# Kernel tuning notes

Measured on AMD Instinct MI355X. Metric: run time of the kernel, lower is better.

## Reference

```python
import jax, jax.numpy as jnp
import numpy as np
from jax import lax

N = 20000          # num_nodes_total
N_GHOST = 2000     # nodes with mask == 0
T_IN = 8
FEAT = 16          # node_features
HID = 128          # hidden_dim
E = 320000         # edges (~avg degree 16)
D = 2              # downstream_concat_depth
ALPHA = 0.5        # alpha_boundary
FUSER_IN = FEAT * (1 + D) + 1   # 49
FUSER_H = max(32, 2 * FEAT * (1 + D))  # 96
GATE_H = max(8, FUSER_H // 2)   # 48


def _lin(k, fan_in, shape):
    b = 1.0 / np.sqrt(fan_in)
    return jax.random.uniform(k, shape, jnp.float32, -b, b)


def setup_inputs() -> dict:
    key = jax.random.key(0)
    ks = jax.random.split(key, 26)
    x = jax.random.normal(ks[0], (N, T_IN, FEAT), jnp.float32)
    src = jax.random.randint(ks[1], (E,), 0, N, jnp.int32)
    dst = jax.random.randint(ks[2], (E,), 0, N, jnp.int32)
    # guarantee every ghost node (ids [0, N_GHOST)) has an outgoing edge to a real node
    src = src.at[:N_GHOST].set(jnp.arange(N_GHOST, dtype=jnp.int32))
    dst = dst.at[:N_GHOST].set(jax.random.randint(ks[3], (N_GHOST,), N_GHOST, N, jnp.int32))
    edge_index = jnp.stack([src, dst])
    edge_attr = jax.random.uniform(ks[4], (E, 1), jnp.float32, minval=0.05, maxval=2.0)
    mask = jnp.concatenate([jnp.zeros(N_GHOST, jnp.int32), jnp.ones(N - N_GHOST, jnp.int32)])
    H3 = 3 * HID
    return dict(
        x=x, edge_attr=edge_attr,
        W_lin=_lin(ks[5], FEAT, (FEAT, HID)), b_lin=_lin(ks[6], FEAT, (HID,)),
        Wc1=_lin(ks[7], HID, (HID, HID)), bc1=jnp.zeros((HID,), jnp.float32),
        Wc2=_lin(ks[8], HID, (HID, HID)), bc2=jnp.zeros((HID,), jnp.float32),
        W_ih=_lin(ks[9], HID, (HID, H3)), b_ih=_lin(ks[10], HID, (H3,)),
        W_hh=_lin(ks[11], HID, (HID, H3)), b_hh=_lin(ks[12], HID, (H3,)),
        Wf1=_lin(ks[13], FUSER_IN, (FUSER_IN, FUSER_H)), bf1=_lin(ks[14], FUSER_IN, (FUSER_H,)),
        Wf2=_lin(ks[15], FUSER_H, (FUSER_H, FEAT)), bf2=_lin(ks[16], FUSER_H, (FEAT,)),
        Wg1=_lin(ks[17], FUSER_IN, (FUSER_IN, GATE_H)), bg1=_lin(ks[18], FUSER_IN, (GATE_H,)),
        Wg2=_lin(ks[19], GATE_H, (GATE_H, 1)), bg2=_lin(ks[20], GATE_H, (1,)),
        edge_index=edge_index, mask=mask,
    )


def _forward(x, edge_attr, W_lin, b_lin, Wc1, bc1, Wc2, bc2, W_ih, b_ih, W_hh, b_hh,
             Wf1, bf1, Wf2, bf2, Wg1, bg1, Wg2, bg2, edge_index, mask):
    src, dst = edge_index[0], edge_index[1]
    ghost_idx = jnp.nonzero(mask == 0, size=N_GHOST)[0]
    dist = jnp.maximum(edge_attr[:, 0], 1e-6)                     # [E]
    # first outgoing edge per source node (earliest edge id per src, cf. argsort trick)
    eid = jnp.arange(E, dtype=jnp.int32)
    first_eid = jax.ops.segment_min(eid, src, num_segments=N)    # int32 max where no edge
    has = first_eid < E
    safe = jnp.where(has, first_eid, 0)
    first_out = jnp.where(has, dst[safe], -1)                     # [N]
    first_dx = jnp.where(has, dist[safe], -1.0)                   # [N]
    b_idx = first_out[ghost_idx]                                  # boundary node per ghost
    dx_bnd = jnp.maximum(first_dx[ghost_idx], 1e-6)[:, None]      # [G,1]
    # D downstream hops, staying put where no outgoing edge exists
    dK, cur = [], b_idx
    for _ in range(D):
        nxt = first_out[cur]
        nxt = jnp.where(nxt < 0, cur, nxt)
        dK.append(nxt)
        cur = nxt
    # GCN symmetric normalization with self-loops (PyG gcn_norm)
    deg = jnp.zeros((N,), x.dtype).at[dst].add(1.0) + 1.0         # in-degree + self-loop
    dis = deg ** -0.5
    norm_e = (dis[src] * dis[dst])[:, None]                       # [E,1]
    norm_self = (1.0 / deg)[:, None]                              # [N,1]

    def gcn(h, W, b):
        hw = h @ W                                                # [N,HID]
        agg = jnp.zeros_like(hw).at[dst].add(hw[src] * norm_e)    # scatter-add messages
        return agg + hw * norm_self + b

    def gru(g, h):
        gi = g @ W_ih + b_ih                                      # [N,3H]
        gh = h @ W_hh + b_hh
        ir, iz, inn = jnp.split(gi, 3, axis=1)
        hr, hz, hn = jnp.split(gh, 3, axis=1)
        r = jax.nn.sigmoid(ir + hr)
        z = jax.nn.sigmoid(iz + hz)
        n = jnp.tanh(inn + r * hn)
        return (1.0 - z) * n + z * h

    def step(h, x_t):
        gf = x_t[ghost_idx]                                       # [G,F]
        feats = jnp.concatenate([gf] + [x_t[i] for i in dK] + [dx_bnd], axis=1)  # [G,FUSER_IN]
        zf = jax.nn.relu(feats @ Wf1 + bf1)
        delta = zf @ Wf2 + bf2
        gate = jax.nn.sigmoid(jax.nn.relu(feats @ Wg1 + bg1) @ Wg2 + bg2)
        x_t = x_t.at[ghost_idx].set(gf + ALPHA * delta * gate)
        g = jax.nn.relu(x_t @ W_lin + b_lin)
        g = jax.nn.relu(gcn(g, Wc1, bc1))
        g = jax.nn.relu(gcn(g, Wc2, bc2))
        return gru(g, h), None

    h0 = jnp.zeros((N, HID), x.dtype)
    h, _ = lax.scan(step, h0, jnp.swapaxes(x, 0, 1))              # scan over T_IN
    return h


def reference(x, edge_attr, W_lin, b_lin, Wc1, bc1, Wc2, bc2, W_ih, b_ih, W_hh, b_hh,
              Wf1, bf1, Wf2, bf2, Wg1, bg1, Wg2, bg2, edge_index, mask):
    return _forward(x, edge_attr, W_lin, b_lin, Wc1, bc1, Wc2, bc2, W_ih, b_ih, W_hh, b_hh,
                    Wf1, bf1, Wf2, bf2, Wg1, bg1, Wg2, bg2, edge_index, mask)
```

## Files before the change

kernel.cpp:

```cpp
#include <hip/hip_runtime.h>
#include <math.h>

#define NN 20000
#define T_IN 8
#define FEAT 16
#define HID 128
#define H3 384
#define FUSER_IN 49
#define FUSER_H 96
#define GATE_H 48
#define ALPHA 0.5f

typedef unsigned short u16;
typedef __attribute__((ext_vector_type(8))) short bf16x8_t;
typedef __attribute__((ext_vector_type(4))) float f32x4_t;

__device__ __forceinline__ float sigmoidf_(float v) { return 1.0f / (1.0f + expf(-v)); }

__device__ __forceinline__ u16 f2b(float v) {
    unsigned u = __float_as_uint(v);
    unsigned r = (u + 0x7fffu + ((u >> 16) & 1u)) >> 16;
    return (u16)r;
}
__device__ __forceinline__ float b2f(u16 u) { return __uint_as_float(((unsigned)u) << 16); }


__global__ void init_kernel(int* first_eid, int* deg_cnt, int* gcount, int n) {
    int i = blockIdx.x * 256 + threadIdx.x;
    if (i < n) { first_eid[i] = 0x7fffffff; deg_cnt[i] = 0; }
    if (i == 0) *gcount = 0;
}

__global__ void edge_pass1(const int* __restrict__ src, const int* __restrict__ dst,
                           int* first_eid, int* deg_cnt, int e) {
    int i = blockIdx.x * 256 + threadIdx.x;
    if (i < e) {
        atomicMin(&first_eid[src[i]], i);
        atomicAdd(&deg_cnt[dst[i]], 1);
    }
}

__global__ void scan1(const int* __restrict__ cnt, int* tmp, int* bsum, int n) {
    __shared__ int buf[256];
    int tid = threadIdx.x;
    int i = blockIdx.x * 256 + tid;
    int v = (i < n) ? cnt[i] : 0;
    buf[tid] = v;
    __syncthreads();
    #pragma unroll
    for (int off = 1; off < 256; off <<= 1) {
        int t = (tid >= off) ? buf[tid - off] : 0;
        __syncthreads();
        buf[tid] += t;
        __syncthreads();
    }
    if (i < n) tmp[i] = buf[tid];
    if (tid == 255) bsum[blockIdx.x] = buf[255];
}

__global__ void scan2(int* bsum, int nb) {
    __shared__ int buf[256];
    int tid = threadIdx.x;
    int v = (tid < nb) ? bsum[tid] : 0;
    buf[tid] = v;
    __syncthreads();
    #pragma unroll
    for (int off = 1; off < 256; off <<= 1) {
        int t = (tid >= off) ? buf[tid - off] : 0;
        __syncthreads();
        buf[tid] += t;
        __syncthreads();
    }
    if (tid < nb) bsum[tid] = buf[tid];
}

__global__ void scan3(const int* __restrict__ cnt, const int* __restrict__ tmp,
                      const int* __restrict__ bsum,
                      int* row_ptr, int* fill_ptr, float* dis, float* norm_self, int n) {
    int i = blockIdx.x * 256 + threadIdx.x;
    if (i >= n) return;
    int pre = (blockIdx.x > 0) ? bsum[blockIdx.x - 1] : 0;
    int incl = tmp[i] + pre;
    int v = cnt[i];
    row_ptr[i + 1] = incl;
    fill_ptr[i] = incl - v;
    float deg = (float)v + 1.0f;
    dis[i] = 1.0f / sqrtf(deg);
    norm_self[i] = 1.0f / deg;
    if (i == 0) row_ptr[0] = 0;
}

__global__ void firsts_kernel(const int* __restrict__ first_eid, const int* __restrict__ dst,
                              const float* __restrict__ edge_attr,
                              int* first_out, float* first_dx, int n, int e) {
    int i = blockIdx.x * 256 + threadIdx.x;
    if (i >= n) return;
    int fe = first_eid[i];
    if (fe < e) {
        first_out[i] = dst[fe];
        first_dx[i] = fmaxf(edge_attr[fe], 1e-6f);
    } else {
        first_out[i] = -1;
        first_dx[i] = -1.0f;
    }
}

__global__ void edge_pass2(const int* __restrict__ src, const int* __restrict__ dst,
                           int* fill_ptr, const float* __restrict__ dis,
                           int* csr_src, float* csr_w, int e) {
    int i = blockIdx.x * 256 + threadIdx.x;
    if (i < e) {
        int d = dst[i], s = src[i];
        int pos = atomicAdd(&fill_ptr[d], 1);
        csr_src[pos] = s;
        csr_w[pos] = dis[s] * dis[d];
    }
}

__global__ void ghost_kernel(const int* __restrict__ mask, const int* __restrict__ first_out,
                             const float* __restrict__ first_dx,
                             int* d1_of, int* d2_of, float* dxb_of,
                             int* ghost_list, int* ghost_pos, int* gcount, int n) {
    int i = blockIdx.x * 256 + threadIdx.x;
    if (i >= n) return;
    if (mask[i] != 0) { ghost_pos[i] = -1; return; }
    int pos = atomicAdd(gcount, 1);
    ghost_list[pos] = i;
    ghost_pos[i] = pos;
    int b = first_out[i];
    float dxb = fmaxf(first_dx[i], 1e-6f);
    int d1, d2;
    if (b < 0) { d1 = i; d2 = i; }
    else {
        int n1 = first_out[b]; d1 = (n1 < 0) ? b : n1;
        int n2 = first_out[d1]; d2 = (n2 < 0) ? d1 : n2;
    }
    d1_of[i] = d1; d2_of[i] = d2; dxb_of[i] = dxb;
}

__global__ void zero2_kernel(float* a, int na, unsigned* b, int nb) {
    int stride = gridDim.x * 256;
    for (int i = blockIdx.x * 256 + threadIdx.x; i < na; i += stride) a[i] = 0.0f;
    for (int i = blockIdx.x * 256 + threadIdx.x; i < nb; i += stride) b[i] = 0u;
}

__global__ __launch_bounds__(256)
void wsplit_kernel(const float* __restrict__ W, u16* BT_hi, u16* BT_lo, int Ncols) {
    __shared__ float tile[32][33];
    int nb = blockIdx.x * 32;
    int kb = blockIdx.y * 32;
    int tx = threadIdx.x & 31, ty = threadIdx.x >> 5;
    #pragma unroll
    for (int r = 0; r < 32; r += 8)
        tile[ty + r][tx] = W[(size_t)(kb + ty + r) * Ncols + nb + tx];
    __syncthreads();
    #pragma unroll
    for (int r = 0; r < 32; r += 8) {
        float v = tile[tx][ty + r];
        u16 h = f2b(v);
        size_t off = (size_t)(nb + ty + r) * 128 + kb + tx;
        BT_hi[off] = h;
        BT_lo[off] = f2b(v - b2f(h));
    }
}


__global__ __launch_bounds__(128)
void fuse_ghost(const float* __restrict__ x,
                const int* __restrict__ ghost_list, const int* __restrict__ gcount,
                const int* __restrict__ d1_of, const int* __restrict__ d2_of,
                const float* __restrict__ dxb_of,
                const float* __restrict__ Wf1, const float* __restrict__ bf1,
                const float* __restrict__ Wf2, const float* __restrict__ bf2,
                const float* __restrict__ Wg1, const float* __restrict__ bg1,
                const float* __restrict__ Wg2, const float* __restrict__ bg2,
                float* __restrict__ xf_buf) {
    int slot = blockIdx.x;
    if (slot >= *gcount) return;
    int t = blockIdx.y;
    int i = ghost_list[slot];
    int j = threadIdx.x;
    __shared__ float feats[FUSER_IN];
    __shared__ float z1[FUSER_H];
    __shared__ float zg[GATE_H];
    __shared__ float s_gate;

    if (j < FEAT) {
        int d1 = d1_of[i], d2 = d2_of[i];
        feats[j]            = x[((size_t)i * T_IN + t) * FEAT + j];
        feats[FEAT + j]     = x[((size_t)d1 * T_IN + t) * FEAT + j];
        feats[2 * FEAT + j] = x[((size_t)d2 * T_IN + t) * FEAT + j];
    }
    if (j == 0) feats[3 * FEAT] = dxb_of[i];
    __syncthreads();
    if (j < FUSER_H) {
        float acc = bf1[j];
        for (int k = 0; k < FUSER_IN; ++k) acc = fmaf(feats[k], Wf1[k * FUSER_H + j], acc);
        z1[j] = fmaxf(acc, 0.0f);
    }
    if (j < GATE_H) {
        float acc = bg1[j];
        for (int k = 0; k < FUSER_IN; ++k) acc = fmaf(feats[k], Wg1[k * GATE_H + j], acc);
        zg[j] = fmaxf(acc, 0.0f);
    }
    __syncthreads();
    if (j == 0) {
        float s = bg2[0];
        for (int k = 0; k < GATE_H; ++k) s = fmaf(zg[k], Wg2[k], s);
        s_gate = sigmoidf_(s);
    }
    __syncthreads();
    if (j < FEAT) {
        float acc = bf2[j];
        for (int k = 0; k < FUSER_H; ++k) acc = fmaf(z1[k], Wf2[k * FEAT + j], acc);
        xf_buf[((size_t)slot * T_IN + t) * FEAT + j] = feats[j] + ALPHA * acc * s_gate;
    }
}

__global__ __launch_bounds__(256)
void lin_all(const float* __restrict__ x, const float* __restrict__ xf_buf,
             const int* __restrict__ ghost_pos,
             const float* __restrict__ W_lin, const float* __restrict__ b_lin,
             u16* __restrict__ g8_hi, u16* __restrict__ g8_lo, int n, int total) {
    __shared__ float Wl[FEAT][HID];
    __shared__ float bl[HID];
    #pragma unroll
    for (int k8 = 0; k8 < 8; ++k8) {
        int idx = threadIdx.x + k8 * 256;
        Wl[idx >> 7][idx & 127] = W_lin[idx];
    }
    if (threadIdx.x < HID) bl[threadIdx.x] = b_lin[threadIdx.x];
    __syncthreads();
    int j = threadIdx.x & 127;
    for (int pair = blockIdx.x * 2 + (threadIdx.x >> 7); pair < total; pair += gridDim.x * 2) {
        int node = pair % n;
        int t = pair / n;
        int gp = ghost_pos[node];
        const float* xr = (gp >= 0) ? &xf_buf[((size_t)gp * T_IN + t) * FEAT]
                                    : &x[((size_t)node * T_IN + t) * FEAT];
        float acc = bl[j];
        #pragma unroll
        for (int k = 0; k < FEAT; ++k) acc = fmaf(xr[k], Wl[k][j], acc);
        float v = fmaxf(acc, 0.0f);
        u16 hv = f2b(v);
        size_t off = (size_t)pair * HID + j;
        g8_hi[off] = hv;
        g8_lo[off] = f2b(v - b2f(hv));
    }
}

__global__ __launch_bounds__(256)
void gemm_gcn_b(const u16* __restrict__ Ahi0, const u16* __restrict__ Alo0,
                const u16* __restrict__ BThi, const u16* __restrict__ BTlo,
                u16* __restrict__ Cb0, int M) {
    constexpr int BM = 64;
    __shared__ u16 ldsA[2][BM * 128];
    const size_t tOff = (size_t)blockIdx.z * M * 128;
    const u16* Ahi = Ahi0 + tOff;
    const u16* Alo = Alo0 + tOff;
    u16*       Cb  = Cb0 + tOff;

    const int tid  = threadIdx.x;
    const int row0 = blockIdx.x * BM;
    constexpr int MF = BM / 32;

    #pragma unroll
    for (int it = 0; it < BM / 16; ++it) {
        int unit = tid + it * 256;
        int r = unit >> 4, s = unit & 15;
        int gr = row0 + r;
        uint4 vh = make_uint4(0, 0, 0, 0), vl = vh;
        if (gr < M) {
            vh = *reinterpret_cast<const uint4*>(&Ahi[(size_t)gr * 128 + s * 8]);
            vl = *reinterpret_cast<const uint4*>(&Alo[(size_t)gr * 128 + s * 8]);
        }
        int byte = (r * 256 + s * 16) ^ ((r & 7) << 4);
        *reinterpret_cast<uint4*>((char*)(&ldsA[0][0]) + byte) = vh;
        *reinterpret_cast<uint4*>((char*)(&ldsA[1][0]) + byte) = vl;
    }
    __syncthreads();

    const int wid  = tid >> 6;
    const int lane = tid & 63;
    const int wr = (wid >> 1) * (BM / 2);
    const int wc = (wid & 1) * 64;
    const int l15 = lane & 15;
    const int lkh = lane >> 4;

    f32x4_t acc[MF][4] = {};

    #pragma unroll
    for (int kb = 0; kb < 4; ++kb) {
        bf16x8_t ah[MF], al[MF], bh[4], bl[4];
        #pragma unroll
        for (int m = 0; m < MF; ++m) {
            int row = wr + m * 16 + l15;
            int byte = (row * 256 + kb * 64 + lkh * 16) ^ ((row & 7) << 4);
            ah[m] = *reinterpret_cast<const bf16x8_t*>((const char*)(&ldsA[0][0]) + byte);
            al[m] = *reinterpret_cast<const bf16x8_t*>((const char*)(&ldsA[1][0]) + byte);
        }
        #pragma unroll
        for (int nf = 0; nf < 4; ++nf) {
            int col = wc + nf * 16 + l15;
            size_t off = (size_t)col * 128 + kb * 32 + lkh * 8;
            bh[nf] = *reinterpret_cast<const bf16x8_t*>(&BThi[off]);
            bl[nf] = *reinterpret_cast<const bf16x8_t*>(&BTlo[off]);
        }
        #pragma unroll
        for (int m = 0; m < MF; ++m)
            #pragma unroll
            for (int nf = 0; nf < 4; ++nf) {
                acc[m][nf] = __builtin_amdgcn_mfma_f32_16x16x32_bf16(ah[m], bh[nf], acc[m][nf], 0, 0, 0);
                acc[m][nf] = __builtin_amdgcn_mfma_f32_16x16x32_bf16(ah[m], bl[nf], acc[m][nf], 0, 0, 0);
                acc[m][nf] = __builtin_amdgcn_mfma_f32_16x16x32_bf16(al[m], bh[nf], acc[m][nf], 0, 0, 0);
            }
    }

    #pragma unroll
    for (int m = 0; m < MF; ++m) {
        int rbase = row0 + wr + m * 16 + lkh * 4;
        #pragma unroll
        for (int nf = 0; nf < 4; ++nf) {
            int col = wc + nf * 16 + l15;
            #pragma unroll
            for (int r2 = 0; r2 < 4; ++r2) {
                int row = rbase + r2;
                if (row < M) Cb[(size_t)row * 128 + col] = f2b(acc[m][nf][r2]);
            }
        }
    }
}

__global__ __launch_bounds__(256)
void gcn_agg_b(const u16* __restrict__ hwb0,
               const int* __restrict__ row_ptr,
               const int* __restrict__ csr_src, const float* __restrict__ csr_w,
               const float* __restrict__ norm_self, const float* __restrict__ bias,
               u16* __restrict__ g_hi0, u16* __restrict__ g_lo0, int n, int nblk) {
    int bid = blockIdx.x;
    int t = bid & 7;
    int q = bid >> 3;
    int blk = q % nblk;
    int half = q / nblk;
    int node = blk * 16 + (threadIdx.x >> 4);
    int lane = threadIdx.x & 15;
    if (node >= n) return;
    const size_t tOff = (size_t)t * n * 128;
    const u16* hwb = hwb0 + tOff;
    u16* g_hi = g_hi0 + tOff;
    u16* g_lo = g_lo0 + tOff;
    const int cb = half * 64 + lane * 4;

    ushort4 sv = *reinterpret_cast<const ushort4*>(&hwb[(size_t)node * HID + cb]);
    float ns = norm_self[node];
    float4 a0, a1, a2, a3;
    a0.x = b2f(sv.x) * ns; a0.y = b2f(sv.y) * ns; a0.z = b2f(sv.z) * ns; a0.w = b2f(sv.w) * ns;
    a1 = make_float4(0.f, 0.f, 0.f, 0.f); a2 = a1; a3 = a1;
    int p  = row_ptr[node];
    int p1 = row_ptr[node + 1];
    for (; p + 4 <= p1; p += 4) {
        int s0 = csr_src[p], s1 = csr_src[p + 1], s2 = csr_src[p + 2], s3 = csr_src[p + 3];
        float w0 = csr_w[p], w1 = csr_w[p + 1], w2 = csr_w[p + 2], w3 = csr_w[p + 3];
        ushort4 v0 = *reinterpret_cast<const ushort4*>(&hwb[(size_t)s0 * HID + cb]);
        ushort4 v1 = *reinterpret_cast<const ushort4*>(&hwb[(size_t)s1 * HID + cb]);
        ushort4 v2 = *reinterpret_cast<const ushort4*>(&hwb[(size_t)s2 * HID + cb]);
        ushort4 v3 = *reinterpret_cast<const ushort4*>(&hwb[(size_t)s3 * HID + cb]);
        a0.x = fmaf(b2f(v0.x), w0, a0.x); a0.y = fmaf(b2f(v0.y), w0, a0.y);
        a0.z = fmaf(b2f(v0.z), w0, a0.z); a0.w = fmaf(b2f(v0.w), w0, a0.w);
        a1.x = fmaf(b2f(v1.x), w1, a1.x); a1.y = fmaf(b2f(v1.y), w1, a1.y);
        a1.z = fmaf(b2f(v1.z), w1, a1.z); a1.w = fmaf(b2f(v1.w), w1, a1.w);
        a2.x = fmaf(b2f(v2.x), w2, a2.x); a2.y = fmaf(b2f(v2.y), w2, a2.y);
        a2.z = fmaf(b2f(v2.z), w2, a2.z); a2.w = fmaf(b2f(v2.w), w2, a2.w);
        a3.x = fmaf(b2f(v3.x), w3, a3.x); a3.y = fmaf(b2f(v3.y), w3, a3.y);
        a3.z = fmaf(b2f(v3.z), w3, a3.z); a3.w = fmaf(b2f(v3.w), w3, a3.w);
    }
    for (; p < p1; ++p) {
        int s = csr_src[p];
        float w = csr_w[p];
        ushort4 v = *reinterpret_cast<const ushort4*>(&hwb[(size_t)s * HID + cb]);
        a0.x = fmaf(b2f(v.x), w, a0.x); a0.y = fmaf(b2f(v.y), w, a0.y);
        a0.z = fmaf(b2f(v.z), w, a0.z); a0.w = fmaf(b2f(v.w), w, a0.w);
    }
    float4 b4 = reinterpret_cast<const float4*>(bias)[half * 16 + lane];
    float ox = fmaxf(a0.x + a1.x + a2.x + a3.x + b4.x, 0.0f);
    float oy = fmaxf(a0.y + a1.y + a2.y + a3.y + b4.y, 0.0f);
    float oz = fmaxf(a0.z + a1.z + a2.z + a3.z + b4.z, 0.0f);
    float ow = fmaxf(a0.w + a1.w + a2.w + a3.w + b4.w, 0.0f);
    ushort4 hv, lv;
    hv.x = f2b(ox); lv.x = f2b(ox - b2f(hv.x));
    hv.y = f2b(oy); lv.y = f2b(oy - b2f(hv.y));
    hv.z = f2b(oz); lv.z = f2b(oz - b2f(hv.z));
    hv.w = f2b(ow); lv.w = f2b(ow - b2f(hv.w));
    *reinterpret_cast<ushort4*>(&g_hi[(size_t)node * HID + cb]) = hv;
    *reinterpret_cast<ushort4*>(&g_lo[(size_t)node * HID + cb]) = lv;
}


__global__ __launch_bounds__(256)
void gru_fused2(const u16* __restrict__ g_hi, const u16* __restrict__ g_lo,
                const u16* __restrict__ h_hi, const u16* __restrict__ h_lo,
                const u16* __restrict__ WihT_hi, const u16* __restrict__ WihT_lo,
                const u16* __restrict__ WhhT_hi, const u16* __restrict__ WhhT_lo,
                const float* __restrict__ b_ih, const float* __restrict__ b_hh,
                float* __restrict__ h, u16* __restrict__ h_hi_o, u16* __restrict__ h_lo_o,
                int n) {
    __shared__ u16 lds[4][32 * 128];
    const int tid  = threadIdx.x;
    const int row0 = blockIdx.x * 32;

    #pragma unroll
    for (int it = 0; it < 2; ++it) {
        int unit = tid + it * 256;
        int r = unit >> 4, s = unit & 15;
        int gr = row0 + r;
        uint4 vg = make_uint4(0,0,0,0), vG = vg, vh = vg, vH = vg;
        if (gr < n) {
            size_t goff = (size_t)gr * 128 + s * 8;
            vg = *reinterpret_cast<const uint4*>(&g_hi[goff]);
            vG = *reinterpret_cast<const uint4*>(&g_lo[goff]);
            vh = *reinterpret_cast<const uint4*>(&h_hi[goff]);
            vH = *reinterpret_cast<const uint4*>(&h_lo[goff]);
        }
        int byte = (r * 256 + s * 16) ^ ((r & 7) << 4);
        *reinterpret_cast<uint4*>((char*)(&lds[0][0]) + byte) = vg;
        *reinterpret_cast<uint4*>((char*)(&lds[1][0]) + byte) = vG;
        *reinterpret_cast<uint4*>((char*)(&lds[2][0]) + byte) = vh;
        *reinterpret_cast<uint4*>((char*)(&lds[3][0]) + byte) = vH;
    }
    __syncthreads();

    const int wid  = tid >> 6;
    const int lane = tid & 63;
    const int l15  = lane & 15;
    const int lkh  = lane >> 4;

    f32x4_t agi[3][2][2] = {};
    f32x4_t agh[3][2][2] = {};

    #pragma unroll
    for (int kb = 0; kb < 4; ++kb) {
        bf16x8_t Agh[2], Agl[2], Ahh[2], Ahl[2];
        #pragma unroll
        for (int m = 0; m < 2; ++m) {
            int row = m * 16 + l15;
            int byte = (row * 256 + kb * 64 + lkh * 16) ^ ((row & 7) << 4);
            Agh[m] = *reinterpret_cast<const bf16x8_t*>((const char*)(&lds[0][0]) + byte);
            Agl[m] = *reinterpret_cast<const bf16x8_t*>((const char*)(&lds[1][0]) + byte);
            Ahh[m] = *reinterpret_cast<const bf16x8_t*>((const char*)(&lds[2][0]) + byte);
            Ahl[m] = *reinterpret_cast<const bf16x8_t*>((const char*)(&lds[3][0]) + byte);
        }
        #pragma unroll
        for (int gt = 0; gt < 3; ++gt) {
            #pragma unroll
            for (int nf = 0; nf < 2; ++nf) {
                int col = gt * HID + wid * 32 + nf * 16 + l15;
                size_t off = (size_t)col * 128 + kb * 32 + lkh * 8;
                bf16x8_t bih = *reinterpret_cast<const bf16x8_t*>(&WihT_hi[off]);
                bf16x8_t bil = *reinterpret_cast<const bf16x8_t*>(&WihT_lo[off]);
                bf16x8_t bhh = *reinterpret_cast<const bf16x8_t*>(&WhhT_hi[off]);
                bf16x8_t bhl = *reinterpret_cast<const bf16x8_t*>(&WhhT_lo[off]);
                #pragma unroll
                for (int m = 0; m < 2; ++m) {
                    agi[gt][m][nf] = __builtin_amdgcn_mfma_f32_16x16x32_bf16(Agh[m], bih, agi[gt][m][nf], 0, 0, 0);
                    agi[gt][m][nf] = __builtin_amdgcn_mfma_f32_16x16x32_bf16(Agh[m], bil, agi[gt][m][nf], 0, 0, 0);
                    agi[gt][m][nf] = __builtin_amdgcn_mfma_f32_16x16x32_bf16(Agl[m], bih, agi[gt][m][nf], 0, 0, 0);
                    agh[gt][m][nf] = __builtin_amdgcn_mfma_f32_16x16x32_bf16(Ahh[m], bhh, agh[gt][m][nf], 0, 0, 0);
                    agh[gt][m][nf] = __builtin_amdgcn_mfma_f32_16x16x32_bf16(Ahh[m], bhl, agh[gt][m][nf], 0, 0, 0);
                    agh[gt][m][nf] = __builtin_amdgcn_mfma_f32_16x16x32_bf16(Ahl[m], bhh, agh[gt][m][nf], 0, 0, 0);
                }
            }
        }
    }

    #pragma unroll
    for (int nf = 0; nf < 2; ++nf) {
        int col = wid * 32 + nf * 16 + l15;
        float bir = b_ih[col], biz = b_ih[HID + col], bin_ = b_ih[2 * HID + col];
        float bhr = b_hh[col], bhz = b_hh[HID + col], bhn = b_hh[2 * HID + col];
        #pragma unroll
        for (int m = 0; m < 2; ++m) {
            #pragma unroll
            for (int r2 = 0; r2 < 4; ++r2) {
                int grow = row0 + m * 16 + lkh * 4 + r2;
                if (grow >= n) continue;
                float rr = sigmoidf_((agi[0][m][nf][r2] + bir) + (agh[0][m][nf][r2] + bhr));
                float zz = sigmoidf_((agi[1][m][nf][r2] + biz) + (agh[1][m][nf][r2] + bhz));
                float nn2 = tanhf((agi[2][m][nf][r2] + bin_) + rr * (agh[2][m][nf][r2] + bhn));
                size_t off = (size_t)grow * HID + col;
                float hold = h[off];
                float hnew = (1.0f - zz) * nn2 + zz * hold;
                h[off] = hnew;
                u16 hv = f2b(hnew);
                h_hi_o[off] = hv;
                h_lo_o[off] = f2b(hnew - b2f(hv));
            }
        }
    }
}


extern "C" void kernel_launch(void* const* d_in, const int* in_sizes, int n_in,
                              void* d_out, int out_size, void* d_ws, size_t ws_size,
                              hipStream_t stream) {
    const float* x        = (const float*)d_in[0];
    const float* edge_attr= (const float*)d_in[1];
    const float* W_lin    = (const float*)d_in[2];
    const float* b_lin    = (const float*)d_in[3];
    const float* Wc1      = (const float*)d_in[4];
    const float* bc1      = (const float*)d_in[5];
    const float* Wc2      = (const float*)d_in[6];
    const float* bc2      = (const float*)d_in[7];
    const float* W_ih     = (const float*)d_in[8];
    const float* b_ih     = (const float*)d_in[9];
    const float* W_hh     = (const float*)d_in[10];
    const float* b_hh     = (const float*)d_in[11];
    const float* Wf1      = (const float*)d_in[12];
    const float* bf1      = (const float*)d_in[13];
    const float* Wf2      = (const float*)d_in[14];
    const float* bf2      = (const float*)d_in[15];
    const float* Wg1      = (const float*)d_in[16];
    const float* bg1      = (const float*)d_in[17];
    const float* Wg2      = (const float*)d_in[18];
    const float* bg2      = (const float*)d_in[19];
    const int*   edge_index = (const int*)d_in[20];
    const int*   mask     = (const int*)d_in[21];

    const int n = in_sizes[21];
    const int e = in_sizes[1];
    const int* src = edge_index;
    const int* dst = edge_index + e;
    float* h = (float*)d_out;

    char* w = (char*)d_ws;
    auto alloc = [&](size_t bytes) -> char* {
        char* p = w;
        w += (bytes + 255) & ~(size_t)255;
        return p;
    };
    int*   first_eid = (int*)  alloc((size_t)n * 4);
    int*   deg_cnt   = (int*)  alloc((size_t)n * 4);
    int*   row_ptr   = (int*)  alloc((size_t)(n + 1) * 4);
    int*   fill_ptr  = (int*)  alloc((size_t)n * 4);
    int*   tmp_scan  = (int*)  alloc((size_t)n * 4);
    int*   bsum      = (int*)  alloc((size_t)256 * 4);
    float* dis       = (float*)alloc((size_t)n * 4);
    float* norm_self = (float*)alloc((size_t)n * 4);
    int*   first_out = (int*)  alloc((size_t)n * 4);
    float* first_dx  = (float*)alloc((size_t)n * 4);
    int*   d1_of     = (int*)  alloc((size_t)n * 4);
    int*   d2_of     = (int*)  alloc((size_t)n * 4);
    float* dxb_of    = (float*)alloc((size_t)n * 4);
    int*   ghost_list= (int*)  alloc((size_t)n * 4);
    int*   ghost_pos = (int*)  alloc((size_t)n * 4);
    int*   gcount    = (int*)  alloc(256);
    int*   csr_src   = (int*)  alloc((size_t)e * 4);
    float* csr_w     = (float*)alloc((size_t)e * 4);
    u16* Wc1T_hi = (u16*)alloc((size_t)HID * 128 * 2);
    u16* Wc1T_lo = (u16*)alloc((size_t)HID * 128 * 2);
    u16* Wc2T_hi = (u16*)alloc((size_t)HID * 128 * 2);
    u16* Wc2T_lo = (u16*)alloc((size_t)HID * 128 * 2);
    u16* WihT_hi = (u16*)alloc((size_t)H3 * 128 * 2);
    u16* WihT_lo = (u16*)alloc((size_t)H3 * 128 * 2);
    u16* WhhT_hi = (u16*)alloc((size_t)H3 * 128 * 2);
    u16* WhhT_lo = (u16*)alloc((size_t)H3 * 128 * 2);
    u16*   g8_hi = (u16*)  alloc((size_t)T_IN * n * HID * 2);
    u16*   g8_lo = (u16*)  alloc((size_t)T_IN * n * HID * 2);
    u16*   bufHb = (u16*)  alloc((size_t)T_IN * n * HID * 2);
    float* xf_buf= (float*)alloc((size_t)n * T_IN * FEAT * 4);
    u16*   h_hi  = (u16*)  alloc((size_t)n * HID * 2);
    u16*   h_lo  = (u16*)  alloc((size_t)n * HID * 2);

    const int TPB = 256;
    const int nb = (n + 255) / 256;
    dim3 gN(nb), gE((e + TPB - 1) / TPB);

    init_kernel<<<gN, TPB, 0, stream>>>(first_eid, deg_cnt, gcount, n);
    edge_pass1<<<gE, TPB, 0, stream>>>(src, dst, first_eid, deg_cnt, e);
    scan1<<<gN, TPB, 0, stream>>>(deg_cnt, tmp_scan, bsum, n);
    scan2<<<1, TPB, 0, stream>>>(bsum, nb);
    scan3<<<gN, TPB, 0, stream>>>(deg_cnt, tmp_scan, bsum, row_ptr, fill_ptr, dis, norm_self, n);
    firsts_kernel<<<gN, TPB, 0, stream>>>(first_eid, dst, edge_attr, first_out, first_dx, n, e);
    edge_pass2<<<gE, TPB, 0, stream>>>(src, dst, fill_ptr, dis, csr_src, csr_w, e);
    ghost_kernel<<<gN, TPB, 0, stream>>>(mask, first_out, first_dx, d1_of, d2_of, dxb_of,
                                         ghost_list, ghost_pos, gcount, n);
    wsplit_kernel<<<dim3(HID / 32, 4), TPB, 0, stream>>>(Wc1, Wc1T_hi, Wc1T_lo, HID);
    wsplit_kernel<<<dim3(HID / 32, 4), TPB, 0, stream>>>(Wc2, Wc2T_hi, Wc2T_lo, HID);
    wsplit_kernel<<<dim3(H3 / 32, 4), TPB, 0, stream>>>(W_ih, WihT_hi, WihT_lo, H3);
    wsplit_kernel<<<dim3(H3 / 32, 4), TPB, 0, stream>>>(W_hh, WhhT_hi, WhhT_lo, H3);

    zero2_kernel<<<2048, TPB, 0, stream>>>(h, n * HID, (unsigned*)h_hi, n * HID);

    fuse_ghost<<<dim3(n, T_IN), 128, 0, stream>>>(x, ghost_list, gcount, d1_of, d2_of, dxb_of,
                                                  Wf1, bf1, Wf2, bf2, Wg1, bg1, Wg2, bg2,
                                                  xf_buf);
    lin_all<<<2048, 256, 0, stream>>>(x, xf_buf, ghost_pos, W_lin, b_lin,
                                      g8_hi, g8_lo, n, n * T_IN);
    dim3 grid_gcn((n + 63) / 64, 1, T_IN);
    const int nblk16 = (n + 15) / 16;
    const int agg_blocks = 2 * 8 * nblk16;
    gemm_gcn_b<<<grid_gcn, 256, 0, stream>>>(g8_hi, g8_lo, Wc1T_hi, Wc1T_lo, bufHb, n);
    gcn_agg_b<<<agg_blocks, 256, 0, stream>>>(bufHb, row_ptr, csr_src, csr_w,
                                              norm_self, bc1, g8_hi, g8_lo, n, nblk16);
    gemm_gcn_b<<<grid_gcn, 256, 0, stream>>>(g8_hi, g8_lo, Wc2T_hi, Wc2T_lo, bufHb, n);
    gcn_agg_b<<<agg_blocks, 256, 0, stream>>>(bufHb, row_ptr, csr_src, csr_w,
                                              norm_self, bc2, g8_hi, g8_lo, n, nblk16);

    const int gru_blocks = (n + 31) / 32;
    for (int t = 0; t < T_IN; ++t) {
        const u16* Gt_hi = g8_hi + (size_t)t * n * HID;
        const u16* Gt_lo = g8_lo + (size_t)t * n * HID;
        gru_fused2<<<gru_blocks, 256, 0, stream>>>(Gt_hi, Gt_lo, h_hi, h_lo,
                                                   WihT_hi, WihT_lo, WhhT_hi, WhhT_lo,
                                                   b_ih, b_hh, h, h_hi, h_lo, n);
    }
}
```

Before: 952.7 us.

## Hoist GRU input projection into one batched GEMM across timesteps

The input-to-hidden GRU projection (g_t @ W_ih) does not depend on the recurrent state, so it is now computed for all 8 timesteps in a single batched MFMA GEMM into an fp32 workspace buffer. The per-step GRU kernel then only does the recurrent W_hh matmul and reads the precomputed gates. This removes half the MFMA work from the serial chain and gives the hoisted GEMM a wide, parallel grid, at the cost of writing and reading about 245 MB of fp32 gate values. Separately, the GCN aggregation now maps one node per 32 lanes covering all 128 columns instead of splitting columns into two halves, which halves the CSR index and weight reads.

```diff
diff --git a/kernel.cpp b/kernel.cpp
--- a/kernel.cpp
+++ b/kernel.cpp
@@ -332,26 +332,104 @@
 }
 
 __global__ __launch_bounds__(256)
+void gemm_gi_b(const u16* __restrict__ Ahi0, const u16* __restrict__ Alo0,
+               const u16* __restrict__ BThi, const u16* __restrict__ BTlo,
+               float* __restrict__ C0, int M) {
+    constexpr int BM = 64;
+    __shared__ u16 ldsA[2][BM * 128];
+    const u16* Ahi = Ahi0 + (size_t)blockIdx.z * M * 128;
+    const u16* Alo = Alo0 + (size_t)blockIdx.z * M * 128;
+    float*     C   = C0 + (size_t)blockIdx.z * M * H3;
+    const int col0 = blockIdx.y * 128;
+
+    const int tid  = threadIdx.x;
+    const int row0 = blockIdx.x * BM;
+    constexpr int MF = BM / 32;
+
+    #pragma unroll
+    for (int it = 0; it < BM / 16; ++it) {
+        int unit = tid + it * 256;
+        int r = unit >> 4, s = unit & 15;
+        int gr = row0 + r;
+        uint4 vh = make_uint4(0, 0, 0, 0), vl = vh;
+        if (gr < M) {
+            vh = *reinterpret_cast<const uint4*>(&Ahi[(size_t)gr * 128 + s * 8]);
+            vl = *reinterpret_cast<const uint4*>(&Alo[(size_t)gr * 128 + s * 8]);
+        }
+        int byte = (r * 256 + s * 16) ^ ((r & 7) << 4);
+        *reinterpret_cast<uint4*>((char*)(&ldsA[0][0]) + byte) = vh;
+        *reinterpret_cast<uint4*>((char*)(&ldsA[1][0]) + byte) = vl;
+    }
+    __syncthreads();
+
+    const int wid  = tid >> 6;
+    const int lane = tid & 63;
+    const int wr = (wid >> 1) * (BM / 2);
+    const int wc = (wid & 1) * 64;
+    const int l15 = lane & 15;
+    const int lkh = lane >> 4;
+
+    f32x4_t acc[MF][4] = {};
+
+    #pragma unroll
+    for (int kb = 0; kb < 4; ++kb) {
+        bf16x8_t ah[MF], al[MF], bh[4], bl[4];
+        #pragma unroll
+        for (int m = 0; m < MF; ++m) {
+            int row = wr + m * 16 + l15;
+            int byte = (row * 256 + kb * 64 + lkh * 16) ^ ((row & 7) << 4);
+            ah[m] = *reinterpret_cast<const bf16x8_t*>((const char*)(&ldsA[0][0]) + byte);
+            al[m] = *reinterpret_cast<const bf16x8_t*>((const char*)(&ldsA[1][0]) + byte);
+        }
+        #pragma unroll
+        for (int nf = 0; nf < 4; ++nf) {
+            int col = col0 + wc + nf * 16 + l15;
+            size_t off = (size_t)col * 128 + kb * 32 + lkh * 8;
+            bh[nf] = *reinterpret_cast<const bf16x8_t*>(&BThi[off]);
+            bl[nf] = *reinterpret_cast<const bf16x8_t*>(&BTlo[off]);
+        }
+        #pragma unroll
+        for (int m = 0; m < MF; ++m)
+            #pragma unroll
+            for (int nf = 0; nf < 4; ++nf) {
+                acc[m][nf] = __builtin_amdgcn_mfma_f32_16x16x32_bf16(ah[m], bh[nf], acc[m][nf], 0, 0, 0);
+                acc[m][nf] = __builtin_amdgcn_mfma_f32_16x16x32_bf16(ah[m], bl[nf], acc[m][nf], 0, 0, 0);
+                acc[m][nf] = __builtin_amdgcn_mfma_f32_16x16x32_bf16(al[m], bh[nf], acc[m][nf], 0, 0, 0);
+            }
+    }
+
+    #pragma unroll
+    for (int m = 0; m < MF; ++m) {
+        int rbase = row0 + wr + m * 16 + lkh * 4;
+        #pragma unroll
+        for (int nf = 0; nf < 4; ++nf) {
+            int col = col0 + wc + nf * 16 + l15;
+            #pragma unroll
+            for (int r2 = 0; r2 < 4; ++r2) {
+                int row = rbase + r2;
+                if (row < M) C[(size_t)row * H3 + col] = acc[m][nf][r2];
+            }
+        }
+    }
+}
+
+__global__ __launch_bounds__(256)
 void gcn_agg_b(const u16* __restrict__ hwb0,
                const int* __restrict__ row_ptr,
                const int* __restrict__ csr_src, const float* __restrict__ csr_w,
                const float* __restrict__ norm_self, const float* __restrict__ bias,
-               u16* __restrict__ g_hi0, u16* __restrict__ g_lo0, int n, int nblk) {
-    int bid = blockIdx.x;
-    int t = bid & 7;
-    int q = bid >> 3;
-    int blk = q % nblk;
-    int half = q / nblk;
-    int node = blk * 16 + (threadIdx.x >> 4);
-    int lane = threadIdx.x & 15;
+               u16* __restrict__ g_hi0, u16* __restrict__ g_lo0, int n) {
+    int t   = blockIdx.x & 7;
+    int blk = blockIdx.x >> 3;
+    int node = blk * 8 + (threadIdx.x >> 5);
+    int lane = threadIdx.x & 31;
     if (node >= n) return;
     const size_t tOff = (size_t)t * n * 128;
     const u16* hwb = hwb0 + tOff;
     u16* g_hi = g_hi0 + tOff;
     u16* g_lo = g_lo0 + tOff;
-    const int cb = half * 64 + lane * 4;
-
-    ushort4 sv = *reinterpret_cast<const ushort4*>(&hwb[(size_t)node * HID + cb]);
+
+    ushort4 sv = *reinterpret_cast<const ushort4*>(&hwb[(size_t)node * HID + lane * 4]);
     float ns = norm_self[node];
     float4 a0, a1, a2, a3;
     a0.x = b2f(sv.x) * ns; a0.y = b2f(sv.y) * ns; a0.z = b2f(sv.z) * ns; a0.w = b2f(sv.w) * ns;
@@ -361,10 +439,10 @@
     for (; p + 4 <= p1; p += 4) {
         int s0 = csr_src[p], s1 = csr_src[p + 1], s2 = csr_src[p + 2], s3 = csr_src[p + 3];
         float w0 = csr_w[p], w1 = csr_w[p + 1], w2 = csr_w[p + 2], w3 = csr_w[p + 3];
-        ushort4 v0 = *reinterpret_cast<const ushort4*>(&hwb[(size_t)s0 * HID + cb]);
-        ushort4 v1 = *reinterpret_cast<const ushort4*>(&hwb[(size_t)s1 * HID + cb]);
-        ushort4 v2 = *reinterpret_cast<const ushort4*>(&hwb[(size_t)s2 * HID + cb]);
-        ushort4 v3 = *reinterpret_cast<const ushort4*>(&hwb[(size_t)s3 * HID + cb]);
+        ushort4 v0 = *reinterpret_cast<const ushort4*>(&hwb[(size_t)s0 * HID + lane * 4]);
+        ushort4 v1 = *reinterpret_cast<const ushort4*>(&hwb[(size_t)s1 * HID + lane * 4]);
+        ushort4 v2 = *reinterpret_cast<const ushort4*>(&hwb[(size_t)s2 * HID + lane * 4]);
+        ushort4 v3 = *reinterpret_cast<const ushort4*>(&hwb[(size_t)s3 * HID + lane * 4]);
         a0.x = fmaf(b2f(v0.x), w0, a0.x); a0.y = fmaf(b2f(v0.y), w0, a0.y);
         a0.z = fmaf(b2f(v0.z), w0, a0.z); a0.w = fmaf(b2f(v0.w), w0, a0.w);
         a1.x = fmaf(b2f(v1.x), w1, a1.x); a1.y = fmaf(b2f(v1.y), w1, a1.y);
@@ -377,11 +455,11 @@
     for (; p < p1; ++p) {
         int s = csr_src[p];
         float w = csr_w[p];
-        ushort4 v = *reinterpret_cast<const ushort4*>(&hwb[(size_t)s * HID + cb]);
+        ushort4 v = *reinterpret_cast<const ushort4*>(&hwb[(size_t)s * HID + lane * 4]);
         a0.x = fmaf(b2f(v.x), w, a0.x); a0.y = fmaf(b2f(v.y), w, a0.y);
         a0.z = fmaf(b2f(v.z), w, a0.z); a0.w = fmaf(b2f(v.w), w, a0.w);
     }
-    float4 b4 = reinterpret_cast<const float4*>(bias)[half * 16 + lane];
+    float4 b4 = reinterpret_cast<const float4*>(bias)[lane];
     float ox = fmaxf(a0.x + a1.x + a2.x + a3.x + b4.x, 0.0f);
     float oy = fmaxf(a0.y + a1.y + a2.y + a3.y + b4.y, 0.0f);
     float oz = fmaxf(a0.z + a1.z + a2.z + a3.z + b4.z, 0.0f);
@@ -391,8 +469,8 @@
     hv.y = f2b(oy); lv.y = f2b(oy - b2f(hv.y));
     hv.z = f2b(oz); lv.z = f2b(oz - b2f(hv.z));
     hv.w = f2b(ow); lv.w = f2b(ow - b2f(hv.w));
-    *reinterpret_cast<ushort4*>(&g_hi[(size_t)node * HID + cb]) = hv;
-    *reinterpret_cast<ushort4*>(&g_lo[(size_t)node * HID + cb]) = lv;
+    *reinterpret_cast<ushort4*>(&g_hi[(size_t)node * HID + lane * 4]) = hv;
+    *reinterpret_cast<ushort4*>(&g_lo[(size_t)node * HID + lane * 4]) = lv;
 }
 
 
@@ -486,6 +564,99 @@
                 float rr = sigmoidf_((agi[0][m][nf][r2] + bir) + (agh[0][m][nf][r2] + bhr));
                 float zz = sigmoidf_((agi[1][m][nf][r2] + biz) + (agh[1][m][nf][r2] + bhz));
                 float nn2 = tanhf((agi[2][m][nf][r2] + bin_) + rr * (agh[2][m][nf][r2] + bhn));
+                size_t off = (size_t)grow * HID + col;
+                float hold = h[off];
+                float hnew = (1.0f - zz) * nn2 + zz * hold;
+                h[off] = hnew;
+                u16 hv = f2b(hnew);
+                h_hi_o[off] = hv;
+                h_lo_o[off] = f2b(hnew - b2f(hv));
+            }
+        }
+    }
+}
+
+__global__ __launch_bounds__(256)
+void gru_fused3(const float* __restrict__ gi8t,
+                const u16* __restrict__ h_hi, const u16* __restrict__ h_lo,
+                const u16* __restrict__ WhhT_hi, const u16* __restrict__ WhhT_lo,
+                const float* __restrict__ b_ih, const float* __restrict__ b_hh,
+                float* __restrict__ h, u16* __restrict__ h_hi_o, u16* __restrict__ h_lo_o,
+                int n) {
+    __shared__ u16 lds[2][32 * 128];
+    const int tid  = threadIdx.x;
+    const int row0 = blockIdx.x * 32;
+
+    #pragma unroll
+    for (int it = 0; it < 2; ++it) {
+        int unit = tid + it * 256;
+        int r = unit >> 4, s = unit & 15;
+        int gr = row0 + r;
+        uint4 vh = make_uint4(0,0,0,0), vH = vh;
+        if (gr < n) {
+            size_t goff = (size_t)gr * 128 + s * 8;
+            vh = *reinterpret_cast<const uint4*>(&h_hi[goff]);
+            vH = *reinterpret_cast<const uint4*>(&h_lo[goff]);
+        }
+        int byte = (r * 256 + s * 16) ^ ((r & 7) << 4);
+        *reinterpret_cast<uint4*>((char*)(&lds[0][0]) + byte) = vh;
+        *reinterpret_cast<uint4*>((char*)(&lds[1][0]) + byte) = vH;
+    }
+    __syncthreads();
+
+    const int wid  = tid >> 6;
+    const int lane = tid & 63;
+    const int l15  = lane & 15;
+    const int lkh  = lane >> 4;
+
+    f32x4_t agh[3][2][2] = {};
+
+    #pragma unroll
+    for (int kb = 0; kb < 4; ++kb) {
+        bf16x8_t Ahh[2], Ahl[2];
+        #pragma unroll
+        for (int m = 0; m < 2; ++m) {
+            int row = m * 16 + l15;
+            int byte = (row * 256 + kb * 64 + lkh * 16) ^ ((row & 7) << 4);
+            Ahh[m] = *reinterpret_cast<const bf16x8_t*>((const char*)(&lds[0][0]) + byte);
+            Ahl[m] = *reinterpret_cast<const bf16x8_t*>((const char*)(&lds[1][0]) + byte);
+        }
+        #pragma unroll
+        for (int gt = 0; gt < 3; ++gt) {
+            #pragma unroll
+            for (int nf = 0; nf < 2; ++nf) {
+                int col = gt * HID + wid * 32 + nf * 16 + l15;
+                size_t off = (size_t)col * 128 + kb * 32 + lkh * 8;
+                bf16x8_t bhh = *reinterpret_cast<const bf16x8_t*>(&WhhT_hi[off]);
+                bf16x8_t bhl = *reinterpret_cast<const bf16x8_t*>(&WhhT_lo[off]);
+                #pragma unroll
+                for (int m = 0; m < 2; ++m) {
+                    agh[gt][m][nf] = __builtin_amdgcn_mfma_f32_16x16x32_bf16(Ahh[m], bhh, agh[gt][m][nf], 0, 0, 0);
+                    agh[gt][m][nf] = __builtin_amdgcn_mfma_f32_16x16x32_bf16(Ahh[m], bhl, agh[gt][m][nf], 0, 0, 0);
+                    agh[gt][m][nf] = __builtin_amdgcn_mfma_f32_16x16x32_bf16(Ahl[m], bhh, agh[gt][m][nf], 0, 0, 0);
+                }
+            }
+        }
+    }
+
+    #pragma unroll
+    for (int nf = 0; nf < 2; ++nf) {
+        int col = wid * 32 + nf * 16 + l15;
+        float bir = b_ih[col], biz = b_ih[HID + col], bin_ = b_ih[2 * HID + col];
+        float bhr = b_hh[col], bhz = b_hh[HID + col], bhn = b_hh[2 * HID + col];
+        #pragma unroll
+        for (int m = 0; m < 2; ++m) {
+            #pragma unroll
+            for (int r2 = 0; r2 < 4; ++r2) {
+                int grow = row0 + m * 16 + lkh * 4 + r2;
+                if (grow >= n) continue;
+                size_t gbase = (size_t)grow * H3 + col;
+                float gir = gi8t[gbase];
+                float giz = gi8t[gbase + HID];
+                float gin = gi8t[gbase + 2 * HID];
+                float rr = sigmoidf_((gir + bir) + (agh[0][m][nf][r2] + bhr));
+                float zz = sigmoidf_((giz + biz) + (agh[1][m][nf][r2] + bhz));
+                float nn2 = tanhf((gin + bin_) + rr * (agh[2][m][nf][r2] + bhn));
                 size_t off = (size_t)grow * HID + col;
                 float hold = h[off];
                 float hnew = (1.0f - zz) * nn2 + zz * hold;
@@ -569,6 +740,10 @@
     float* xf_buf= (float*)alloc((size_t)n * T_IN * FEAT * 4);
     u16*   h_hi  = (u16*)  alloc((size_t)n * HID * 2);
     u16*   h_lo  = (u16*)  alloc((size_t)n * HID * 2);
+    size_t gi8_bytes = (size_t)T_IN * n * H3 * 4;
+    size_t used = (size_t)(w - (char*)d_ws);
+    bool use_gi8 = (used + gi8_bytes + 256) <= ws_size;
+    float* gi8 = use_gi8 ? (float*)alloc(gi8_bytes) : nullptr;
 
     const int TPB = 256;
     const int nb = (n + 255) / 256;
@@ -596,21 +771,31 @@
     lin_all<<<2048, 256, 0, stream>>>(x, xf_buf, ghost_pos, W_lin, b_lin,
                                       g8_hi, g8_lo, n, n * T_IN);
     dim3 grid_gcn((n + 63) / 64, 1, T_IN);
-    const int nblk16 = (n + 15) / 16;
-    const int agg_blocks = 2 * 8 * nblk16;
+    const int agg_blocks = ((n + 7) / 8) * T_IN;
     gemm_gcn_b<<<grid_gcn, 256, 0, stream>>>(g8_hi, g8_lo, Wc1T_hi, Wc1T_lo, bufHb, n);
     gcn_agg_b<<<agg_blocks, 256, 0, stream>>>(bufHb, row_ptr, csr_src, csr_w,
-                                              norm_self, bc1, g8_hi, g8_lo, n, nblk16);
+                                              norm_self, bc1, g8_hi, g8_lo, n);
     gemm_gcn_b<<<grid_gcn, 256, 0, stream>>>(g8_hi, g8_lo, Wc2T_hi, Wc2T_lo, bufHb, n);
     gcn_agg_b<<<agg_blocks, 256, 0, stream>>>(bufHb, row_ptr, csr_src, csr_w,
-                                              norm_self, bc2, g8_hi, g8_lo, n, nblk16);
+                                              norm_self, bc2, g8_hi, g8_lo, n);
 
     const int gru_blocks = (n + 31) / 32;
-    for (int t = 0; t < T_IN; ++t) {
-        const u16* Gt_hi = g8_hi + (size_t)t * n * HID;
-        const u16* Gt_lo = g8_lo + (size_t)t * n * HID;
-        gru_fused2<<<gru_blocks, 256, 0, stream>>>(Gt_hi, Gt_lo, h_hi, h_lo,
-                                                   WihT_hi, WihT_lo, WhhT_hi, WhhT_lo,
-                                                   b_ih, b_hh, h, h_hi, h_lo, n);
-    }
-}
+    if (use_gi8) {
+        dim3 grid_gi((n + 63) / 64, 3, T_IN);
+        gemm_gi_b<<<grid_gi, 256, 0, stream>>>(g8_hi, g8_lo, WihT_hi, WihT_lo, gi8, n);
+        for (int t = 0; t < T_IN; ++t) {
+            const float* gi8t = gi8 + (size_t)t * n * H3;
+            gru_fused3<<<gru_blocks, 256, 0, stream>>>(gi8t, h_hi, h_lo,
+                                                       WhhT_hi, WhhT_lo,
+                                                       b_ih, b_hh, h, h_hi, h_lo, n);
+        }
+    } else {
+        for (int t = 0; t < T_IN; ++t) {
+            const u16* Gt_hi = g8_hi + (size_t)t * n * HID;
+            const u16* Gt_lo = g8_lo + (size_t)t * n * HID;
+            gru_fused2<<<gru_blocks, 256, 0, stream>>>(Gt_hi, Gt_lo, h_hi, h_lo,
+                                                       WihT_hi, WihT_lo, WhhT_hi, WhhT_lo,
+                                                       b_ih, b_hh, h, h_hi, h_lo, n);
+        }
+    }
+}
```

Result: no change. 934.6 us (-1.9%).
